# Kernel tuning notes

Hardware: AMD Instinct MI355X
Metric: run time of the kernel (lower is better)

The kernel has to match this reference:

```python
import jax, jax.numpy as jnp
import numpy as np

B, N, Hh, E = 16, 1024, 8, 64      # q/k/v: (B, N, H, E), H*E == ich
C, K, ICH, MODES = 64, 8, 512, 16  # c, k, ich, modes
IN_CH, OUT_CH, LVL = 64, 64, 0     # in_channels, out_channels, L


def fourier_cross_attn(q, k, v):
    """FourierCrossAttentionW with activation='tanh'. q,k,v: (B,L,E,H) -> (B,L,E,H).
    mode_select indices are range(min(L//2, modes)) -> contiguous low-mode slice.
    Note: v is unused in the original (only its length, equal to k's here)."""
    L = q.shape[1]
    xq = jnp.transpose(q, (0, 3, 2, 1))  # (B,H,E,L)
    xk = jnp.transpose(k, (0, 3, 2, 1))
    m = min(L // 2, MODES)
    xq_ft = jnp.fft.rfft(xq, axis=-1)[..., :m]   # (B,H,E,m) complex
    xk_ft = jnp.fft.rfft(xk, axis=-1)[..., :m]
    xqk = jnp.tanh(jnp.einsum('bhex,bhey->bhxy', xq_ft, xk_ft))  # complex tanh, (B,H,m,m)
    xqkv = jnp.einsum('bhxy,bhey->bhex', xqk, xk_ft)             # (B,H,E,m)
    pad = jnp.zeros(xqkv.shape[:-1] + (L // 2 + 1 - m,), xqkv.dtype)
    out_ft = jnp.concatenate([xqkv, pad], axis=-1)               # scatter low modes, rest zero
    out = jnp.fft.irfft(out_ft / (IN_CH * OUT_CH), n=L, axis=-1)
    return jnp.transpose(out, (0, 3, 2, 1))


def wavelet_transform(x, ec_d, ec_s):
    # x: (B, L, c, k) -> detail, approx each (B, L//2, c, k)
    xa = jnp.concatenate([x[:, ::2], x[:, 1::2]], axis=-1)  # (B, L/2, c, 2k)
    return xa @ ec_d, xa @ ec_s


def even_odd(x, rc_e, rc_o):
    # x: (B, L, c, 2k) -> (B, 2L, c, k), interleaving even/odd reconstructions
    b, n, c, _ = x.shape
    x_e = x @ rc_e  # (B,L,c,k)
    x_o = x @ rc_o
    return jnp.stack([x_e, x_o], axis=2).reshape(b, 2 * n, c, K)


def _forward(q, k, v, Lq_w, Lq_b, Lk_w, Lk_b, Lv_w, Lv_b, out_w, out_b,
             ec_s, ec_d, rc_e, rc_o):
    b, n, _, _ = q.shape
    s = k.shape[1]
    q = (q.reshape(b, n, ICH) @ Lq_w + Lq_b).reshape(b, n, C, K)
    k = (k.reshape(b, s, ICH) @ Lk_w + Lk_b).reshape(b, s, C, K)
    v = (v.reshape(b, s, ICH) @ Lv_w + Lv_b).reshape(b, s, C, K)
    if n > s:
        z = jnp.zeros((b, n - s, C, K), q.dtype)
        v = jnp.concatenate([v, z], axis=1)
        k = jnp.concatenate([k, z], axis=1)
    else:
        v = v[:, :n]
        k = k[:, :n]
    ns = int(np.floor(np.log2(n)))
    nl = 2 ** int(np.ceil(np.log2(n)))
    if nl > n:  # pad to power of two by wrapping leading entries
        q = jnp.concatenate([q, q[:, :nl - n]], axis=1)
        k = jnp.concatenate([k, k[:, :nl - n]], axis=1)
        v = jnp.concatenate([v, v[:, :nl - n]], axis=1)
    Ud, Us = [], []
    for _ in range(ns - LVL):
        dq, q = wavelet_transform(q, ec_d, ec_s)
        dk, k = wavelet_transform(k, ec_d, ec_s)
        dv, v = wavelet_transform(v, ec_d, ec_s)
        # original: attn1(d_q,d_k,d_v) + attn2(s_q,s_k,s_v); Us uses details (Us_q stores d)
        Ud.append(fourier_cross_attn(dq, dk, dv) + fourier_cross_attn(q, k, v))
        Us.append(fourier_cross_attn(dq, dk, dv))
    v = fourier_cross_attn(q, k, v)
    for i in range(ns - 1 - LVL, -1, -1):
        v = v + Us[i]
        v = jnp.concatenate([v, Ud[i]], axis=-1)
        v = even_odd(v, rc_e, rc_o)
    return v[:, :n].reshape(b, n, C * K) @ out_w + out_b


def setup_inputs() -> dict:
    key = jax.random.key(0)
    ks = jax.random.split(key, 16)
    f = jax.random.normal
    ws = 1.0 / np.sqrt(ICH)       # Linear init scale
    fs = 1.0 / np.sqrt(2 * K)     # wavelet filter scale (stand-in for legendre filters)
    return {
        'q': f(ks[0], (B, N, Hh, E), jnp.float32),
        'k': f(ks[1], (B, N, Hh, E), jnp.float32),
        'v': f(ks[2], (B, N, Hh, E), jnp.float32),
        'Lq_w': f(ks[3], (ICH, C * K), jnp.float32) * ws,
        'Lq_b': f(ks[4], (C * K,), jnp.float32) * ws,
        'Lk_w': f(ks[5], (ICH, C * K), jnp.float32) * ws,
        'Lk_b': f(ks[6], (C * K,), jnp.float32) * ws,
        'Lv_w': f(ks[7], (ICH, C * K), jnp.float32) * ws,
        'Lv_b': f(ks[8], (C * K,), jnp.float32) * ws,
        'out_w': f(ks[9], (C * K, ICH), jnp.float32) * ws,
        'out_b': f(ks[10], (ICH,), jnp.float32) * ws,
        'ec_s': f(ks[11], (2 * K, K), jnp.float32) * fs,
        'ec_d': f(ks[12], (2 * K, K), jnp.float32) * fs,
        'rc_e': f(ks[13], (2 * K, K), jnp.float32) * fs,
        'rc_o': f(ks[14], (2 * K, K), jnp.float32) * fs,
    }


def reference(q, k, v, Lq_w, Lq_b, Lk_w, Lk_b, Lv_w, Lv_b, out_w, out_b,
              ec_s, ec_d, rc_e, rc_o):
    return _forward(q, k, v, Lq_w, Lq_b, Lk_w, Lk_b, Lv_w, Lv_b,
                    out_w, out_b, ec_s, ec_d, rc_e, rc_o)
```

## Files before the change

kernel.cpp:

```cpp
#include <hip/hip_runtime.h>
#include <cstddef>

#define PI2F 6.283185307179586f

typedef __bf16 bf16_t;
typedef __bf16 bf16x8 __attribute__((ext_vector_type(8)));
typedef float f32x4 __attribute__((ext_vector_type(4)));

#define QA_OFF   0u
#define KA_OFF   8388608u
#define CH_OFF   16777216u
#define MF_OFF   (CH_OFF + 33488896u)
#define MUS_OFF  (MF_OFF + 9437184u)
#define MUD_OFF  (MUS_OFF + 2359296u)
#define WF_OFF   (MUD_OFF + 2359296u)
#define WI_OFF   (WF_OFF + 32704u)

__global__ __launch_bounds__(256)
void wprep_k(const float* __restrict__ Wq, const float* __restrict__ Wk,
             const float* __restrict__ Wo, bf16_t* __restrict__ WT)
{
    __shared__ float T[32][33];
    const int w = blockIdx.x >> 8;
    const int tile = blockIdx.x & 255;
    const int k0 = (tile & 15) * 32, n0 = (tile >> 4) * 32;
    const float* W = (w == 0) ? Wq : (w == 1) ? Wk : Wo;
    bf16_t* oh = WT + (size_t)w * 524288;
    bf16_t* ol = oh + 262144;
    const int tid = threadIdx.x;
    {
        int row = tid >> 3, q = tid & 7;
        float4 v = *(const float4*)(W + (size_t)(k0 + row) * 512 + n0 + q * 4);
        T[row][q*4+0] = v.x; T[row][q*4+1] = v.y; T[row][q*4+2] = v.z; T[row][q*4+3] = v.w;
    }
    __syncthreads();
    {
        int nr = tid >> 3, q = tid & 7;
        union { bf16_t b[4]; uint2 u; } ph, pl;
#pragma unroll
        for (int j = 0; j < 4; ++j) {
            float x = T[q*4+j][nr];
            bf16_t h = (bf16_t)x;
            ph.b[j] = h;
            pl.b[j] = (bf16_t)(x - (float)h);
        }
        size_t dst = (size_t)(n0 + nr) * 512 + k0 + q * 4;
        *(uint2*)&oh[dst] = ph.u;
        *(uint2*)&ol[dst] = pl.u;
    }
}

template<bool TOUT>
__global__ __launch_bounds__(256)
void mfma_gemm_k(const float* __restrict__ X, const bf16_t* __restrict__ WTh,
                 const bf16_t* __restrict__ WTl, const float* __restrict__ bias,
                 float* __restrict__ out)
{
    __shared__ __align__(16) char smem[40960];
    bf16_t* Ah = (bf16_t*)smem;
    bf16_t* Al = Ah + 128 * 40;
    bf16_t* Bh = Al + 128 * 40;
    bf16_t* Bl = Bh + 128 * 40;
    float* Cs = (float*)smem;
    const int tid = threadIdx.x;
    const int lane = tid & 63;
    const int wv = tid >> 6;
    const int wm = wv & 1, wn = wv >> 1;
    const int m0 = blockIdx.x << 7, n0 = blockIdx.y << 7;
    const int l15 = lane & 15, quad = lane >> 4;

    f32x4 acc[4][4];
    f32x4 zz = {0.f, 0.f, 0.f, 0.f};
#pragma unroll
    for (int i = 0; i < 4; ++i)
#pragma unroll
        for (int j = 0; j < 4; ++j) acc[i][j] = zz;

    for (int kc = 0; kc < 16; ++kc) {
#pragma unroll
        for (int i = 0; i < 4; ++i) {
            int u = tid + i * 256;
            int row = u >> 3, seg = u & 7;
            float4 v = *(const float4*)(X + (size_t)(m0 + row) * 512 + kc * 32 + seg * 4);
            union { bf16_t b[4]; uint2 u2; } ph, pl;
            float xs[4] = {v.x, v.y, v.z, v.w};
#pragma unroll
            for (int j = 0; j < 4; ++j) {
                bf16_t h = (bf16_t)xs[j];
                ph.b[j] = h;
                pl.b[j] = (bf16_t)(xs[j] - (float)h);
            }
            *(uint2*)&Ah[row * 40 + seg * 4] = ph.u2;
            *(uint2*)&Al[row * 40 + seg * 4] = pl.u2;
        }
#pragma unroll
        for (int i = 0; i < 4; ++i) {
            int u = tid + i * 256;
            int variant = u >> 9;
            int rs = u & 511;
            int row = rs >> 2, seg = rs & 3;
            const bf16_t* src = (variant ? WTl : WTh) + (size_t)(n0 + row) * 512 + kc * 32 + seg * 8;
            bf16_t* dst = (variant ? Bl : Bh) + row * 40 + seg * 8;
            *(float4*)dst = *(const float4*)src;
        }
        __syncthreads();
        bf16x8 ah[4], al[4];
#pragma unroll
        for (int mi = 0; mi < 4; ++mi) {
            int row = wm * 64 + mi * 16 + l15;
            ah[mi] = *(bf16x8*)&Ah[row * 40 + quad * 8];
            al[mi] = *(bf16x8*)&Al[row * 40 + quad * 8];
        }
#pragma unroll
        for (int ni = 0; ni < 4; ++ni) {
            int nr = wn * 64 + ni * 16 + l15;
            bf16x8 bh = *(bf16x8*)&Bh[nr * 40 + quad * 8];
            bf16x8 bl = *(bf16x8*)&Bl[nr * 40 + quad * 8];
#pragma unroll
            for (int mi = 0; mi < 4; ++mi) {
                acc[mi][ni] = __builtin_amdgcn_mfma_f32_16x16x32_bf16(ah[mi], bh, acc[mi][ni], 0, 0, 0);
                acc[mi][ni] = __builtin_amdgcn_mfma_f32_16x16x32_bf16(ah[mi], bl, acc[mi][ni], 0, 0, 0);
                acc[mi][ni] = __builtin_amdgcn_mfma_f32_16x16x32_bf16(al[mi], bh, acc[mi][ni], 0, 0, 0);
            }
        }
        __syncthreads();
    }

    if constexpr (TOUT) {
        const int b8 = (m0 >> 10) * 8, tb = m0 & 1023;
        for (int p = 0; p < 2; ++p) {
            if (wn == p) {
#pragma unroll
                for (int ni = 0; ni < 4; ++ni)
#pragma unroll
                    for (int mi = 0; mi < 4; ++mi)
#pragma unroll
                        for (int r = 0; r < 4; ++r) {
                            int nl = ni * 16 + l15;
                            int m = wm * 64 + mi * 16 + quad * 4 + r;
                            Cs[nl * 132 + m] = acc[mi][ni][r];
                        }
            }
            __syncthreads();
#pragma unroll
            for (int i = 0; i < 8; ++i) {
                int u = tid + i * 256;
                int col = u >> 5, seg = u & 31;
                int gc = n0 + p * 64 + col;
                float bz = bias[gc];
                float4 v = *(float4*)&Cs[col * 132 + seg * 4];
                v.x += bz; v.y += bz; v.z += bz; v.w += bz;
                int h = gc & 7, e = gc >> 3;
                *(float4*)(out + (((size_t)(b8 + h)) * 64 + e) * 1024 + tb + seg * 4) = v;
            }
            __syncthreads();
        }
    } else {
#pragma unroll
        for (int ni = 0; ni < 4; ++ni) {
            int n = n0 + wn * 64 + ni * 16 + l15;
            float bz = bias[n];
#pragma unroll
            for (int mi = 0; mi < 4; ++mi)
#pragma unroll
                for (int r = 0; r < 4; ++r) {
                    int m = m0 + wm * 64 + mi * 16 + quad * 4 + r;
                    out[(size_t)m * 512 + n] = acc[mi][ni][r] + bz;
                }
        }
    }
}

__global__ __launch_bounds__(256)
void twiddle_k(float* __restrict__ Wf, float* __restrict__ Wi)
{
    int idx = blockIdx.x * 256 + threadIdx.x;
    int table = idx / 32704;
    if (table >= 2) return;
    int r = idx - table * 32704;
    int lvl = 0, base = 0;
    for (int l = 0; l < 9; ++l) {
        int Ll = 512 >> l;
        int sz = 32 * Ll;
        if (r < base + sz) { lvl = l; break; }
        base += sz;
    }
    int L = 512 >> lvl;
    int rr = r - base;
    if (table == 0) {
        int t = rr >> 5, c = rr & 31;
        int j = c & 15, isIm = c >> 4;
        int mv = (j * t) & (L - 1);
        float ang = (PI2F / (float)L) * (float)mv;
        float s, cc; sincosf(ang, &s, &cc);
        Wf[r] = isIm ? -s : cc;
    } else {
        int k = rr / L, t = rr - (rr / L) * L;
        int j = k & 15, isIm = k >> 4;
        int mv = (j * t) & (L - 1);
        float ang = (PI2F / (float)L) * (float)mv;
        float s, cc; sincosf(ang, &s, &cc);
        float scale = 1.f / (4096.f * (float)L);
        float v;
        if (!isIm) v = (j == 0) ? 1.f : 2.f * cc;
        else       v = (j == 0) ? 0.f : -2.f * s;
        Wi[r] = v * scale;
    }
}

__global__ __launch_bounds__(256)
void wavelet_chain_k(const float* __restrict__ qin, const float* __restrict__ kin,
                     float* __restrict__ CH,
                     const float* __restrict__ ecd, const float* __restrict__ ecs)
{
    __shared__ float bufA[8][1032];
    __shared__ float bufB[8][520];
    __shared__ float bufD[8][520];
    __shared__ float fd[128], fs[128];
    const int tid = threadIdx.x;
    const int tensor = blockIdx.x >> 10;
    const int b = (blockIdx.x >> 6) & 15;
    const int e = blockIdx.x & 63;
    const float* in = tensor ? kin : qin;
    if (tid < 128) fd[tid] = ecd[tid];
    else fs[tid - 128] = ecs[tid - 128];

    for (int u = tid; u < 2048; u += 256) {
        int h = u >> 8, q4 = u & 255;
        *(float4*)&bufA[h][q4 * 4] =
            *(const float4*)(in + ((size_t)((b*8 + h) * 64 + e)) * 1024 + q4 * 4);
    }
    __syncthreads();

    float* cur = &bufA[0][0]; int cs = 1032;
    float* pD = &bufD[0][0];
    for (int lvl = 0; lvl < 9; ++lvl) {
        const int L = 512 >> lvl;
        float* sOut; int ss;
        if (cur == &bufA[0][0]) { sOut = &bufB[0][0]; ss = 520; }
        else                    { sOut = &bufA[0][0]; ss = 1032; }

        for (int t = tid; t < L; t += 256) {
            float xa[16];
#pragma unroll
            for (int h = 0; h < 8; ++h) {
                xa[h]     = cur[h * cs + 2 * t];
                xa[8 + h] = cur[h * cs + 2 * t + 1];
            }
#pragma unroll
            for (int jj = 0; jj < 8; ++jj) {
                float ad = 0.f, as_ = 0.f;
#pragma unroll
                for (int rr = 0; rr < 16; ++rr) {
                    ad  = fmaf(xa[rr], fd[rr * 8 + jj], ad);
                    as_ = fmaf(xa[rr], fs[rr * 8 + jj], as_);
                }
                pD[jj * 520 + t]  = ad;
                sOut[jj * ss + t] = as_;
            }
        }
        __syncthreads();

        const size_t chb = (size_t)32768 * (size_t)(1024 - 2 * L);
        if (L >= 4) {
            const int nv = 4 * L;
            for (int u = tid; u < nv; u += 256) {
                int u4 = u * 4;
                int p = u4 / (8 * L);
                int rem = u4 - p * 8 * L;
                int h = rem / L;
                int t4 = rem - h * L;
                float4 v = p ? *(float4*)(sOut + h * ss + t4)
                             : *(float4*)(pD + h * 520 + t4);
                size_t row = (size_t)((tensor * 2 + p) * 8192) + (size_t)(b*8 + h) * 64 + e;
                *(float4*)(CH + chb + row * (size_t)L + t4) = v;
            }
        } else {
            for (int u = tid; u < 16 * L; u += 256) {
                int p = u / (8 * L);
                int rem = u - p * 8 * L;
                int h = rem / L;
                int t = rem - h * L;
                float v = p ? sOut[h * ss + t] : pD[h * 520 + t];
                size_t row = (size_t)((tensor * 2 + p) * 8192) + (size_t)(b*8 + h) * 64 + e;
                CH[chb + row * (size_t)L + t] = v;
            }
        }
        __syncthreads();
        cur = sOut; cs = ss;
    }
}

__global__ __launch_bounds__(256)
void fwd_dft_k(const float* __restrict__ CH, const float* __restrict__ Wf,
               float* __restrict__ MF)
{
    __shared__ float As[32][132];
    __shared__ float Ws[32][36];
    const int tid = threadIdx.x;
    const int lvl = blockIdx.x >> 8;
    const int tile = blockIdx.x & 255;
    const int L = 512 >> lvl;
    const size_t chb = (size_t)32768 * (size_t)(1024 - 2 * L);
    const int wb = 32 * (1024 - 2 * L);
    const size_t mfb = (size_t)lvl * 1048576;
    const int rowb = tile * 128;
    const int rg = tid >> 3, cg = tid & 7;
    float acc[4][4] = {{0.f}};
    const int kw = (L < 32) ? L : 32;

    for (int k0 = 0; k0 < L; k0 += kw) {
        if (kw >= 4) {
            const int kq = kw >> 2;
            const int kqs = (kq == 8) ? 3 : (kq == 4) ? 2 : (kq == 2) ? 1 : 0;
            const int nf4 = 128 * kq;
            for (int u = tid; u < nf4; u += 256) {
                int row = u >> kqs, q = u & (kq - 1);
                float4 v = *(const float4*)(CH + chb + (size_t)(rowb + row) * L + k0 + q * 4);
                As[q*4+0][row] = v.x; As[q*4+1][row] = v.y;
                As[q*4+2][row] = v.z; As[q*4+3][row] = v.w;
            }
        } else {
            if (tid < 256) {
                int row = tid >> 1, t = tid & 1;
                As[t][row] = CH[chb + (size_t)(rowb + row) * 2 + t];
            }
        }
        for (int u = tid; u < kw * 8; u += 256) {
            int kr = u >> 3, q = u & 7;
            *(float4*)&Ws[kr][q * 4] = *(const float4*)&Wf[wb + (k0 + kr) * 32 + q * 4];
        }
        __syncthreads();
#pragma unroll 4
        for (int kk = 0; kk < kw; ++kk) {
            float4 a4 = *(float4*)&As[kk][rg * 4];
            float4 w4 = *(float4*)&Ws[kk][cg * 4];
            acc[0][0] = fmaf(a4.x, w4.x, acc[0][0]); acc[0][1] = fmaf(a4.x, w4.y, acc[0][1]);
            acc[0][2] = fmaf(a4.x, w4.z, acc[0][2]); acc[0][3] = fmaf(a4.x, w4.w, acc[0][3]);
            acc[1][0] = fmaf(a4.y, w4.x, acc[1][0]); acc[1][1] = fmaf(a4.y, w4.y, acc[1][1]);
            acc[1][2] = fmaf(a4.y, w4.z, acc[1][2]); acc[1][3] = fmaf(a4.y, w4.w, acc[1][3]);
            acc[2][0] = fmaf(a4.z, w4.x, acc[2][0]); acc[2][1] = fmaf(a4.z, w4.y, acc[2][1]);
            acc[2][2] = fmaf(a4.z, w4.z, acc[2][2]); acc[2][3] = fmaf(a4.z, w4.w, acc[2][3]);
            acc[3][0] = fmaf(a4.w, w4.x, acc[3][0]); acc[3][1] = fmaf(a4.w, w4.y, acc[3][1]);
            acc[3][2] = fmaf(a4.w, w4.z, acc[3][2]); acc[3][3] = fmaf(a4.w, w4.w, acc[3][3]);
        }
        __syncthreads();
    }
#pragma unroll
    for (int i = 0; i < 4; ++i) {
        float4 o = {acc[i][0], acc[i][1], acc[i][2], acc[i][3]};
        *(float4*)(MF + mfb + (size_t)(rowb + rg * 4 + i) * 32 + cg * 4) = o;
    }
}

__global__ __launch_bounds__(256)
void combine2_k(const float* __restrict__ MF, float* __restrict__ MUS, float* __restrict__ MUD)
{
    __shared__ float F[4][64][33];
    __shared__ float Sre[2][16][17], Sim[2][16][17];
    const int tid = threadIdx.x;
    const int lvl = blockIdx.x >> 7;
    const int bh = blockIdx.x & 127;
    const int L = 512 >> lvl;
    const int m = (L / 2 < 16) ? L / 2 : 16;
    const size_t mfb = (size_t)lvl * 1048576;
    for (int a = 0; a < 4; ++a) {
        const float* src = MF + mfb + ((size_t)a * 8192 + (size_t)bh * 64) * 32;
        for (int u = tid; u < 512; u += 256) {
            float4 v = *(const float4*)(src + u * 4);
            int ee = (u * 4) >> 5, c = (u * 4) & 31;
            F[a][ee][c] = v.x; F[a][ee][c+1] = v.y; F[a][ee][c+2] = v.z; F[a][ee][c+3] = v.w;
        }
    }
    __syncthreads();
    const int mm = m * m;
    for (int idx = tid; idx < 2 * mm; idx += 256) {
        int p = idx / mm, rr = idx - p * mm;
        int x = rr / m, y = rr - (rr / m) * m;
        float sr = 0.f, si = 0.f;
        for (int ee = 0; ee < 64; ++ee) {
            float qre = F[p][ee][x],     qim = F[p][ee][16 + x];
            float kre = F[2 + p][ee][y], kim = F[2 + p][ee][16 + y];
            sr = fmaf(qre, kre, sr); sr = fmaf(-qim, kim, sr);
            si = fmaf(qre, kim, si); si = fmaf(qim, kre, si);
        }
        float twoa = fminf(fmaxf(2.f * sr, -30.f), 30.f);
        float e2 = expf(twoa), inv = 1.f / e2;
        float s2b, c2b; sincosf(2.f * si, &s2b, &c2b);
        float den = 0.5f * (e2 + inv) + c2b;
        Sre[p][x][y] = 0.5f * (e2 - inv) / den;
        Sim[p][x][y] = s2b / den;
    }
    __syncthreads();
    for (int idx = tid; idx < 1024; idx += 256) {
        int ee = idx >> 4, x = idx & 15;
        float urd = 0.f, uid = 0.f, urs = 0.f, uis = 0.f;
        if (x < m) {
            for (int y = 0; y < m; ++y) {
                float k0re = F[2][ee][y], k0im = F[2][ee][16 + y];
                float k1re = F[3][ee][y], k1im = F[3][ee][16 + y];
                float s0r = Sre[0][x][y], s0i = Sim[0][x][y];
                float s1r = Sre[1][x][y], s1i = Sim[1][x][y];
                urd = fmaf(s0r, k0re, urd); urd = fmaf(-s0i, k0im, urd);
                uid = fmaf(s0r, k0im, uid); uid = fmaf(s0i, k0re, uid);
                urs = fmaf(s1r, k1re, urs); urs = fmaf(-s1i, k1im, urs);
                uis = fmaf(s1r, k1im, uis); uis = fmaf(s1i, k1re, uis);
            }
        }
        size_t mb = (size_t)lvl * 262144 + ((size_t)bh * 64 + ee) * 32;
        MUS[mb + x]      = urd;
        MUS[mb + 16 + x] = uid;
        MUD[mb + x]      = urd + urs;
        MUD[mb + 16 + x] = uid + uis;
    }
}

__global__ __launch_bounds__(256)
void inv_dft_k(const float* __restrict__ MUS, const float* __restrict__ MUD,
               const float* __restrict__ Wi,
               float* __restrict__ US, float* __restrict__ UD)
{
    __shared__ float As[32][132];
    __shared__ float Ws[32][36];
    const int bx = blockIdx.x;
    int lvl = 0, base = 0;
#pragma unroll
    for (int l = 0; l < 9; ++l) {
        int cl = 128 << ((l <= 4) ? (4 - l) : 0);
        if (bx < base + cl) { lvl = l; break; }
        base += cl;
    }
    const int r = bx - base;
    const int L = 512 >> lvl;
    const int tcb = (lvl <= 4) ? (4 - lvl) : 0;
    const int tile = r >> tcb;
    const int tc = r & ((1 << tcb) - 1);
    const int t0 = tc * 32;
    const int ar = tile >> 6;
    const int rowb = (tile & 63) * 128;
    const float* MU = ar ? MUD : MUS;
    float* OUT = ar ? UD : US;
    const int wb = 32 * (1024 - 2 * L);
    const size_t uoff = (size_t)8192 * (size_t)(1024 - 2 * L);
    const int nc = (L < 32) ? L : 32;
    const int tid = threadIdx.x;
    const int rg = tid >> 3, cg = tid & 7;

#pragma unroll
    for (int i = 0; i < 4; ++i) {
        int u = tid + i * 256;
        int row = u >> 3, q = u & 7;
        float4 v = *(const float4*)(MU + (size_t)lvl * 262144 + (size_t)(rowb + row) * 32 + q * 4);
        As[q*4+0][row] = v.x; As[q*4+1][row] = v.y;
        As[q*4+2][row] = v.z; As[q*4+3][row] = v.w;
    }
    if (L >= 4) {
        int ncq = nc >> 2;
        int bits = (nc == 32) ? 3 : (nc == 16) ? 2 : (nc == 8) ? 1 : 0;
        for (int u = tid; u < 32 * ncq; u += 256) {
            int kr = u >> bits, q = u & (ncq - 1);
            *(float4*)&Ws[kr][q * 4] = *(const float4*)&Wi[wb + kr * L + t0 + q * 4];
        }
    } else {
        for (int u = tid; u < 64; u += 256)
            Ws[u >> 1][u & 1] = Wi[wb + (u >> 1) * 2 + (u & 1)];
    }
    __syncthreads();
    if (cg * 4 < nc) {
        float acc[4][4] = {{0.f}};
#pragma unroll 8
        for (int kk = 0; kk < 32; ++kk) {
            float4 a4 = *(float4*)&As[kk][rg * 4];
            float4 w4 = *(float4*)&Ws[kk][cg * 4];
            acc[0][0] = fmaf(a4.x, w4.x, acc[0][0]); acc[0][1] = fmaf(a4.x, w4.y, acc[0][1]);
            acc[0][2] = fmaf(a4.x, w4.z, acc[0][2]); acc[0][3] = fmaf(a4.x, w4.w, acc[0][3]);
            acc[1][0] = fmaf(a4.y, w4.x, acc[1][0]); acc[1][1] = fmaf(a4.y, w4.y, acc[1][1]);
            acc[1][2] = fmaf(a4.y, w4.z, acc[1][2]); acc[1][3] = fmaf(a4.y, w4.w, acc[1][3]);
            acc[2][0] = fmaf(a4.z, w4.x, acc[2][0]); acc[2][1] = fmaf(a4.z, w4.y, acc[2][1]);
            acc[2][2] = fmaf(a4.z, w4.z, acc[2][2]); acc[2][3] = fmaf(a4.z, w4.w, acc[2][3]);
            acc[3][0] = fmaf(a4.w, w4.x, acc[3][0]); acc[3][1] = fmaf(a4.w, w4.y, acc[3][1]);
            acc[3][2] = fmaf(a4.w, w4.z, acc[3][2]); acc[3][3] = fmaf(a4.w, w4.w, acc[3][3]);
        }
        if (L >= 4) {
#pragma unroll
            for (int i = 0; i < 4; ++i) {
                float4 o = {acc[i][0], acc[i][1], acc[i][2], acc[i][3]};
                *(float4*)(OUT + uoff + (size_t)(rowb + rg * 4 + i) * L + t0 + cg * 4) = o;
            }
        } else {
#pragma unroll
            for (int i = 0; i < 4; ++i) {
                OUT[uoff + (size_t)(rowb + rg * 4 + i) * 2 + 0] = acc[i][0];
                OUT[uoff + (size_t)(rowb + rg * 4 + i) * 2 + 1] = acc[i][1];
            }
        }
    }
}

__global__ __launch_bounds__(256)
void recon_all_k(const float* __restrict__ USg, const float* __restrict__ UDg,
                 const float* __restrict__ rce, const float* __restrict__ rco,
                 float* __restrict__ vT)
{
    __shared__ float v[8][1032];
    __shared__ float se[16][8];
    __shared__ float so[16][8];
    const int tid = threadIdx.x;
    const int b = blockIdx.x >> 6;
    const int e = blockIdx.x & 63;
    if (tid < 128) se[tid >> 3][tid & 7] = rce[tid];
    else { int u = tid - 128; so[u >> 3][u & 7] = rco[u]; }
    if (tid < 16) v[tid >> 1][tid & 1] = 0.f;
    __syncthreads();

    for (int i = 8; i >= 0; --i) {
        const int L = 512 >> i;
        const size_t uoff = (size_t)8192 * (1024 - 2 * L);
        const int nC = (L + 255) >> 8;
        for (int c = nC - 1; c >= 0; --c) {
            const int t = (c << 8) + tid;
            float a[16];
            const bool act = t < L;
            if (act) {
#pragma unroll
                for (int h = 0; h < 8; ++h) {
                    size_t pgl = uoff + ((size_t)((b*8 + h) * 64 + e)) * (size_t)L + t;
                    a[h]     = v[h][t] + USg[pgl];
                    a[8 + h] = UDg[pgl];
                }
            }
            __syncthreads();
            if (act) {
#pragma unroll
                for (int jj = 0; jj < 8; ++jj) {
                    float ev = 0.f, od = 0.f;
#pragma unroll
                    for (int rr = 0; rr < 16; ++rr) {
                        ev = fmaf(a[rr], se[rr][jj], ev);
                        od = fmaf(a[rr], so[rr][jj], od);
                    }
                    v[jj][2 * t]     = ev;
                    v[jj][2 * t + 1] = od;
                }
            }
            __syncthreads();
        }
    }
    for (int u = tid; u < 2048; u += 256) {
        int h = u >> 8, q4 = u & 255;
        float4 val = *(float4*)&v[h][q4 * 4];
        *(float4*)(vT + ((size_t)((b*8 + h) * 64 + e)) * 1024 + q4 * 4) = val;
    }
}

__global__ __launch_bounds__(256)
void trans_tn_k(const float* __restrict__ vT, float* __restrict__ vN)
{
    __shared__ float Ls[512][17];
    const int b = blockIdx.x >> 6;
    const int t0 = (blockIdx.x & 63) << 4;
    const int tid = threadIdx.x;
#pragma unroll
    for (int it = 0; it < 8; ++it) {
        int u = it * 256 + tid;
        int row = u >> 2, part = u & 3;
        float4 v = *(const float4*)(vT + ((size_t)b * 512 + row) * 1024 + t0 + part * 4);
        Ls[row][part*4+0] = v.x;
        Ls[row][part*4+1] = v.y;
        Ls[row][part*4+2] = v.z;
        Ls[row][part*4+3] = v.w;
    }
    __syncthreads();
#pragma unroll
    for (int it = 0; it < 8; ++it) {
        int u = it * 256 + tid;
        int cq = u & 127, tt = u >> 7;
        int c = cq * 4;
        float4 v;
        v.x = Ls[(((c+0) & 7) << 6) + ((c+0) >> 3)][tt];
        v.y = Ls[(((c+1) & 7) << 6) + ((c+1) >> 3)][tt];
        v.z = Ls[(((c+2) & 7) << 6) + ((c+2) >> 3)][tt];
        v.w = Ls[(((c+3) & 7) << 6) + ((c+3) >> 3)][tt];
        *(float4*)(vN + ((size_t)b * 1024 + t0 + tt) * 512 + c) = v;
    }
}

extern "C" void kernel_launch(void* const* d_in, const int* in_sizes, int n_in,
                              void* d_out, int out_size, void* d_ws, size_t ws_size,
                              hipStream_t stream)
{
    const float* q    = (const float*)d_in[0];
    const float* k    = (const float*)d_in[1];
    const float* Lq_w = (const float*)d_in[3];
    const float* Lq_b = (const float*)d_in[4];
    const float* Lk_w = (const float*)d_in[5];
    const float* Lk_b = (const float*)d_in[6];
    const float* outw = (const float*)d_in[9];
    const float* outb = (const float*)d_in[10];
    const float* ec_s = (const float*)d_in[11];
    const float* ec_d = (const float*)d_in[12];
    const float* rc_e = (const float*)d_in[13];
    const float* rc_o = (const float*)d_in[14];

    float* ws = (float*)d_ws;
    float* qA  = ws + QA_OFF;
    float* kA  = ws + KA_OFF;
    float* CH  = ws + CH_OFF;
    float* MF  = ws + MF_OFF;
    float* MUS = ws + MUS_OFF;
    float* MUD = ws + MUD_OFF;
    float* Wf  = ws + WF_OFF;
    float* Wi  = ws + WI_OFF;
    float* vT  = CH;
    float* vN  = CH + 8388608;
    bf16_t* WT = (bf16_t*)MF;

    twiddle_k<<<256, 256, 0, stream>>>(Wf, Wi);
    wprep_k<<<768, 256, 0, stream>>>(Lq_w, Lk_w, outw, WT);

    dim3 gg(128, 4);
    mfma_gemm_k<true><<<gg, 256, 0, stream>>>(q, WT, WT + 262144, Lq_b, qA);
    mfma_gemm_k<true><<<gg, 256, 0, stream>>>(k, WT + 524288, WT + 786432, Lk_b, kA);

    wavelet_chain_k<<<2048, 256, 0, stream>>>(qA, kA, CH, ec_d, ec_s);
    fwd_dft_k<<<2304, 256, 0, stream>>>(CH, Wf, MF);
    combine2_k<<<1152, 256, 0, stream>>>(MF, MUS, MUD);

    wprep_k<<<768, 256, 0, stream>>>(Lq_w, Lk_w, outw, WT);
    inv_dft_k<<<4480, 256, 0, stream>>>(MUS, MUD, Wi, qA, kA);
    recon_all_k<<<1024, 256, 0, stream>>>(qA, kA, rc_e, rc_o, vT);
    trans_tn_k<<<1024, 256, 0, stream>>>(vT, vN);
    mfma_gemm_k<false><<<gg, 256, 0, stream>>>(vN, WT + 1048576, WT + 1310720, outb, (float*)d_out);
}
```

Baseline: 565.3 us.

## Stream wavelet level-0 from global and drop redundant weight re-preparation

The wavelet chain kernel now reads level-0 input straight from global memory and writes detail and approximation coefficients directly to the CH buffer. This removes the large staging buffer and the separate shared-memory copy-out pass, and shrinks LDS so more blocks can be resident per CU. The transposed bf16 weights move to their own workspace region instead of aliasing MF, so the second wprep launch is no longer needed. The trade-off is scalar, strided global stores in place of float4 stores, and the workspace must be large enough for the extra region.

After: 575.1 us. No clear change (+1.7%).

```diff
diff --git a/kernel.cpp b/kernel.cpp
--- a/kernel.cpp
+++ b/kernel.cpp
@@ -15,6 +15,7 @@
 #define MUD_OFF  (MUS_OFF + 2359296u)
 #define WF_OFF   (MUD_OFF + 2359296u)
 #define WI_OFF   (WF_OFF + 32704u)
+#define WT_OFF   (WI_OFF + 32704u)
 
 __global__ __launch_bounds__(256)
 void wprep_k(const float* __restrict__ Wq, const float* __restrict__ Wk,
@@ -213,9 +214,8 @@
                      float* __restrict__ CH,
                      const float* __restrict__ ecd, const float* __restrict__ ecs)
 {
-    __shared__ float bufA[8][1032];
-    __shared__ float bufB[8][520];
-    __shared__ float bufD[8][520];
+    __shared__ float sA[8][520];
+    __shared__ float sB[8][264];
     __shared__ float fd[128], fs[128];
     const int tid = threadIdx.x;
     const int tensor = blockIdx.x >> 10;
@@ -224,28 +224,20 @@
     const float* in = tensor ? kin : qin;
     if (tid < 128) fd[tid] = ecd[tid];
     else fs[tid - 128] = ecs[tid - 128];
-
-    for (int u = tid; u < 2048; u += 256) {
-        int h = u >> 8, q4 = u & 255;
-        *(float4*)&bufA[h][q4 * 4] =
-            *(const float4*)(in + ((size_t)((b*8 + h) * 64 + e)) * 1024 + q4 * 4);
-    }
-    __syncthreads();
-
-    float* cur = &bufA[0][0]; int cs = 1032;
-    float* pD = &bufD[0][0];
-    for (int lvl = 0; lvl < 9; ++lvl) {
-        const int L = 512 >> lvl;
-        float* sOut; int ss;
-        if (cur == &bufA[0][0]) { sOut = &bufB[0][0]; ss = 520; }
-        else                    { sOut = &bufA[0][0]; ss = 1032; }
-
-        for (int t = tid; t < L; t += 256) {
+    __syncthreads();
+
+    const size_t rowd0 = (size_t)((tensor * 2 + 0) * 8192) + (size_t)(b * 8) * 64 + e;
+
+    {
+        const int L = 512;
+#pragma unroll
+        for (int it = 0; it < 2; ++it) {
+            const int t = tid + it * 256;
             float xa[16];
 #pragma unroll
             for (int h = 0; h < 8; ++h) {
-                xa[h]     = cur[h * cs + 2 * t];
-                xa[8 + h] = cur[h * cs + 2 * t + 1];
+                float2 v = *(const float2*)(in + ((size_t)((b*8 + h) * 64 + e)) * 1024 + 2 * t);
+                xa[h] = v.x; xa[8 + h] = v.y;
             }
 #pragma unroll
             for (int jj = 0; jj < 8; ++jj) {
@@ -255,39 +247,45 @@
                     ad  = fmaf(xa[rr], fd[rr * 8 + jj], ad);
                     as_ = fmaf(xa[rr], fs[rr * 8 + jj], as_);
                 }
-                pD[jj * 520 + t]  = ad;
-                sOut[jj * ss + t] = as_;
+                size_t rowd = rowd0 + (size_t)jj * 64;
+                CH[rowd * L + t]          = ad;
+                CH[(rowd + 8192) * L + t] = as_;
+                sA[jj][t] = as_;
+            }
+        }
+    }
+    __syncthreads();
+
+    float* cur = &sA[0][0]; int cs = 520;
+    float* nxt = &sB[0][0]; int ns = 264;
+    for (int lvl = 1; lvl < 9; ++lvl) {
+        const int L = 512 >> lvl;
+        const size_t chb = (size_t)32768 * (size_t)(1024 - 2 * L);
+        if (tid < L) {
+            const int t = tid;
+            float xa[16];
+#pragma unroll
+            for (int h = 0; h < 8; ++h) {
+                xa[h]     = cur[h * cs + 2 * t];
+                xa[8 + h] = cur[h * cs + 2 * t + 1];
+            }
+#pragma unroll
+            for (int jj = 0; jj < 8; ++jj) {
+                float ad = 0.f, as_ = 0.f;
+#pragma unroll
+                for (int rr = 0; rr < 16; ++rr) {
+                    ad  = fmaf(xa[rr], fd[rr * 8 + jj], ad);
+                    as_ = fmaf(xa[rr], fs[rr * 8 + jj], as_);
+                }
+                size_t rowd = rowd0 + (size_t)jj * 64;
+                CH[chb + rowd * L + t]          = ad;
+                CH[chb + (rowd + 8192) * L + t] = as_;
+                nxt[jj * ns + t] = as_;
             }
         }
         __syncthreads();
-
-        const size_t chb = (size_t)32768 * (size_t)(1024 - 2 * L);
-        if (L >= 4) {
-            const int nv = 4 * L;
-            for (int u = tid; u < nv; u += 256) {
-                int u4 = u * 4;
-                int p = u4 / (8 * L);
-                int rem = u4 - p * 8 * L;
-                int h = rem / L;
-                int t4 = rem - h * L;
-                float4 v = p ? *(float4*)(sOut + h * ss + t4)
-                             : *(float4*)(pD + h * 520 + t4);
-                size_t row = (size_t)((tensor * 2 + p) * 8192) + (size_t)(b*8 + h) * 64 + e;
-                *(float4*)(CH + chb + row * (size_t)L + t4) = v;
-            }
-        } else {
-            for (int u = tid; u < 16 * L; u += 256) {
-                int p = u / (8 * L);
-                int rem = u - p * 8 * L;
-                int h = rem / L;
-                int t = rem - h * L;
-                float v = p ? sOut[h * ss + t] : pD[h * 520 + t];
-                size_t row = (size_t)((tensor * 2 + p) * 8192) + (size_t)(b*8 + h) * 64 + e;
-                CH[chb + row * (size_t)L + t] = v;
-            }
-        }
-        __syncthreads();
-        cur = sOut; cs = ss;
+        float* tp = cur; cur = nxt; nxt = tp;
+        int ts_ = cs; cs = ns; ns = ts_;
     }
 }
 
@@ -611,9 +609,9 @@
     float* MUD = ws + MUD_OFF;
     float* Wf  = ws + WF_OFF;
     float* Wi  = ws + WI_OFF;
+    bf16_t* WT = (bf16_t*)(ws + WT_OFF);
     float* vT  = CH;
     float* vN  = CH + 8388608;
-    bf16_t* WT = (bf16_t*)MF;
 
     twiddle_k<<<256, 256, 0, stream>>>(Wf, Wi);
     wprep_k<<<768, 256, 0, stream>>>(Lq_w, Lk_w, outw, WT);
@@ -625,8 +623,6 @@
     wavelet_chain_k<<<2048, 256, 0, stream>>>(qA, kA, CH, ec_d, ec_s);
     fwd_dft_k<<<2304, 256, 0, stream>>>(CH, Wf, MF);
     combine2_k<<<1152, 256, 0, stream>>>(MF, MUS, MUD);
-
-    wprep_k<<<768, 256, 0, stream>>>(Lq_w, Lk_w, outw, WT);
     inv_dft_k<<<4480, 256, 0, stream>>>(MUS, MUD, Wi, qA, kA);
     recon_all_k<<<1024, 256, 0, stream>>>(qA, kA, rc_e, rc_o, vT);
     trans_tn_k<<<1024, 256, 0, stream>>>(vT, vN);
```
